# Performance work log

Hardware: AMD Instinct MI355X
Metric: run time of the kernel (lower is better)

The kernel has to match this reference:

```python
import jax, jax.numpy as jnp
import numpy as np

N = 100000   # nodes
E = 3200000  # edges (avg degree 32)
D_IN = 128
C = 64
EPS = 1e-5  # GraphNorm eps (PyG default)


def _graph_norm(x, alpha, gamma, beta):
    # GraphNorm over a single graph: all N nodes form one segment.
    mean = jnp.mean(x, axis=0, keepdims=True)            # [1, C]
    xc = x - alpha * mean                                # learnable mean-scale
    var = jnp.mean(xc * xc, axis=0, keepdims=True)       # [1, C]
    return gamma * xc * jax.lax.rsqrt(var + EPS) + beta


def _gcn_conv(x, W, bias, src, dst, dinv):
    # GCN with implicit self-loops: out = D^-1/2 (A+I) D^-1/2 (x W) + b
    xw = x @ W                                           # [N, C]
    coef = (dinv[src] * dinv[dst])[:, None]              # [E, 1]
    msg = xw[src] * coef                                 # [E, C] gather
    agg = jax.ops.segment_sum(msg, dst, num_segments=N)  # [N, C] scatter
    agg = agg + xw * (dinv * dinv)[:, None]              # self-loop term
    return agg + bias


def setup_inputs() -> dict:
    key = jax.random.key(0)
    ks = jax.random.split(key, 4)
    x = jax.random.normal(ks[0], (N, D_IN), dtype=jnp.float32)
    edge_index = jax.random.randint(ks[1], (2, E), 0, N, dtype=jnp.int64)
    W0 = jax.random.normal(ks[2], (D_IN, C), dtype=jnp.float32) * (1.0 / np.sqrt(D_IN))
    Ws = jax.random.normal(ks[3], (2, C, C), dtype=jnp.float32) * (1.0 / np.sqrt(C))
    b = jnp.zeros((3, C), dtype=jnp.float32)
    alpha = jnp.ones((3, C), dtype=jnp.float32)
    gamma = jnp.ones((3, C), dtype=jnp.float32)
    beta = jnp.zeros((3, C), dtype=jnp.float32)
    return {"x": x, "edge_index": edge_index, "W0": W0, "Ws": Ws,
            "b": b, "alpha": alpha, "gamma": gamma, "beta": beta}


def reference(x, edge_index, W0, Ws, b, alpha, gamma, beta):
    src, dst = edge_index[0], edge_index[1]
    deg = 1.0 + jax.ops.segment_sum(jnp.ones((E,), dtype=x.dtype), dst, num_segments=N)
    dinv = jax.lax.rsqrt(deg)                            # [N]
    h = _gcn_conv(x, W0, b[0], src, dst, dinv)
    h = _graph_norm(h, alpha[0], gamma[0], beta[0])      # dropout = identity (eval)
    for i in range(2):
        h = _gcn_conv(h, Ws[i], b[i + 1], src, dst, dinv)
        h = _graph_norm(h, alpha[i + 1], gamma[i + 1], beta[i + 1])
    return h
```

## Files before the change

kernel.cpp:

```cpp
#include <hip/hip_runtime.h>
#include <hip/hip_bf16.h>


#define EPS 1e-5f

__device__ __forceinline__ float bf_lo(unsigned u) {
    union { unsigned u; float f; } c; c.u = u << 16; return c.f;
}
__device__ __forceinline__ float bf_hi(unsigned u) {
    union { unsigned u; float f; } c; c.u = u & 0xffff0000u; return c.f;
}
__device__ __forceinline__ unsigned pack_bf2(float a, float b) {
    union { __hip_bfloat16 h; unsigned short u; } ca, cb;
    ca.h = __float2bfloat16(a);
    cb.h = __float2bfloat16(b);
    return (unsigned)ca.u | ((unsigned)cb.u << 16);
}

__global__ __launch_bounds__(256) void k_hist(const int* __restrict__ dst, int* __restrict__ hist,
                                              int E, int SEG, int NBKT) {
    __shared__ int h[2048];
    int t = threadIdx.x;
    for (int b = t; b < NBKT; b += 256) h[b] = 0;
    __syncthreads();
    int i0 = blockIdx.x * SEG, i1 = min(E, i0 + SEG);
    for (int i = i0 + t * 4; i < i1; i += 1024) {
        if (i + 3 < i1) {
            int4 d = *(const int4*)(dst + i);
            atomicAdd(&h[d.x >> 6], 1);
            atomicAdd(&h[d.y >> 6], 1);
            atomicAdd(&h[d.z >> 6], 1);
            atomicAdd(&h[d.w >> 6], 1);
        } else {
            for (int q = i; q < i1; ++q) atomicAdd(&h[dst[q] >> 6], 1);
        }
    }
    __syncthreads();
    for (int b = t; b < NBKT; b += 256) hist[blockIdx.x * NBKT + b] = h[b];
}

__global__ __launch_bounds__(256) void k_scanA(const int* __restrict__ hist, int* __restrict__ chunkScan,
                                               int* __restrict__ chunkTot, int NBKT, int SCAN_N) {
    __shared__ int ls[256];
    int t = threadIdx.x;
    int base = blockIdx.x * 1024 + t * 4;
    int v[4];
#pragma unroll
    for (int j = 0; j < 4; ++j) {
        int l = base + j;
        v[j] = 0;
        if (l < SCAN_N) {
            int blk = l & 255, bkt = l >> 8;
            v[j] = hist[blk * NBKT + bkt];
        }
    }
    int s = v[0] + v[1] + v[2] + v[3];
    ls[t] = s;
    __syncthreads();
    for (int off = 1; off < 256; off <<= 1) {
        int val = (t >= off) ? ls[t - off] : 0;
        __syncthreads();
        ls[t] += val;
        __syncthreads();
    }
    int run = ls[t] - s;
#pragma unroll
    for (int j = 0; j < 4; ++j) {
        chunkScan[base + j] = run;
        run += v[j];
    }
    if (t == 255) chunkTot[blockIdx.x] = ls[255];
}

__global__ void k_scanB(const int* __restrict__ chunkTot, int* __restrict__ chunkBase, int NCH) {
    __shared__ int s[512];
    int t = threadIdx.x;
    s[t] = (t < NCH) ? chunkTot[t] : 0;
    s[t + 256] = (t + 256 < NCH) ? chunkTot[t + 256] : 0;
    __syncthreads();
    for (int off = 1; off < 512; off <<= 1) {
        int a0 = (t >= off) ? s[t - off] : 0;
        int a1 = (t + 256 >= off) ? s[t + 256 - off] : 0;
        __syncthreads();
        s[t] += a0;
        s[t + 256] += a1;
        __syncthreads();
    }
    if (t < NCH) chunkBase[t] = t ? s[t - 1] : 0;
    if (t + 256 < NCH) chunkBase[t + 256] = s[t + 255];
}

__global__ __launch_bounds__(256) void k_scatter_part(const int* __restrict__ src, const int* __restrict__ dst,
                                                      const int* __restrict__ chunkScan,
                                                      const int* __restrict__ chunkBase,
                                                      int* __restrict__ packed, int E, int SEG, int NBKT) {
    __shared__ int cur[2048];
    int blk = blockIdx.x, t = threadIdx.x;
    for (int b = t; b < NBKT; b += 256) {
        int l = b * 256 + blk;
        cur[b] = chunkScan[l] + chunkBase[l >> 10];
    }
    __syncthreads();
    int i0 = blk * SEG, i1 = min(E, i0 + SEG);
    for (int i = i0 + t * 4; i < i1; i += 1024) {
        if (i + 3 < i1) {
            int4 d = *(const int4*)(dst + i);
            int4 s = *(const int4*)(src + i);
            int p;
            p = atomicAdd(&cur[d.x >> 6], 1); packed[p] = (int)(((unsigned)(d.x & 63) << 26) | (unsigned)s.x);
            p = atomicAdd(&cur[d.y >> 6], 1); packed[p] = (int)(((unsigned)(d.y & 63) << 26) | (unsigned)s.y);
            p = atomicAdd(&cur[d.z >> 6], 1); packed[p] = (int)(((unsigned)(d.z & 63) << 26) | (unsigned)s.z);
            p = atomicAdd(&cur[d.w >> 6], 1); packed[p] = (int)(((unsigned)(d.w & 63) << 26) | (unsigned)s.w);
        } else {
            for (int q = i; q < i1; ++q) {
                int dd = dst[q];
                int p = atomicAdd(&cur[dd >> 6], 1);
                packed[p] = (int)(((unsigned)(dd & 63) << 26) | (unsigned)src[q]);
            }
        }
    }
}

__global__ __launch_bounds__(256) void k_ellfill(const int* __restrict__ packed,
                                                 const int* __restrict__ chunkScan,
                                                 const int* __restrict__ chunkBase,
                                                 int* __restrict__ ell, int* __restrict__ cursor,
                                                 float* __restrict__ dinv,
                                                 int CAP, int NBKT, int N, int E) {
    __shared__ int ellLoc[64 * 96];
    __shared__ int cnt[64];
    int bkt = blockIdx.x, t = threadIdx.x;
    if (t < 64) cnt[t] = 0;
    __syncthreads();
    int l0 = bkt * 256;
    int bs = chunkScan[l0] + chunkBase[l0 >> 10];
    int be = E;
    if (bkt + 1 < NBKT) {
        int l1 = (bkt + 1) * 256;
        be = chunkScan[l1] + chunkBase[l1 >> 10];
    }
    for (int i = bs + t; i < be; i += 256) {
        unsigned p = (unsigned)packed[i];
        int s = (int)(p & 0x03FFFFFFu);
        int ld = (int)(p >> 26);
        int slot = atomicAdd(&cnt[ld], 1);
        if (slot < CAP) ellLoc[ld * CAP + slot] = s;
    }
    __syncthreads();
    int lo = bkt << 6;
    int total = 64 * CAP;
    for (int idx = t; idx < total; idx += 256) {
        int ld = idx / CAP;
        int s = idx - ld * CAP;
        if (lo + ld < N && s < min(cnt[ld], CAP))
            ell[(size_t)lo * CAP + idx] = ellLoc[idx];
    }
    if (t < 64 && lo + t < N) {
        int dg = min(cnt[t], CAP);
        cursor[lo + t] = (lo + t) * CAP + dg;
        dinv[lo + t] = rsqrtf(1.0f + (float)cnt[t]);
    }
}

__global__ __launch_bounds__(256) void k_cursor_init(int* cursor, int CAP, int n) {
    int i = blockIdx.x * 256 + threadIdx.x;
    if (i < n) cursor[i] = i * CAP;
}

__global__ __launch_bounds__(256) void k_fill_ell(const int* __restrict__ src, const int* __restrict__ dst,
                                                  int* cursor, int* __restrict__ ell, int E,
                                                  int lo, int hi) {
    int i = (blockIdx.x * 256 + threadIdx.x) * 4;
    if (i + 3 < E) {
        int4 d = *(const int4*)(dst + i);
        int4 s = *(const int4*)(src + i);
        if (d.x >= lo && d.x < hi) ell[atomicAdd(&cursor[d.x], 1)] = s.x;
        if (d.y >= lo && d.y < hi) ell[atomicAdd(&cursor[d.y], 1)] = s.y;
        if (d.z >= lo && d.z < hi) ell[atomicAdd(&cursor[d.z], 1)] = s.z;
        if (d.w >= lo && d.w < hi) ell[atomicAdd(&cursor[d.w], 1)] = s.w;
    } else {
        for (int t = i; t < E; ++t) {
            int d = dst[t];
            if (d >= lo && d < hi) ell[atomicAdd(&cursor[d], 1)] = src[t];
        }
    }
}

__global__ __launch_bounds__(256) void k_deg_dinv(const int* __restrict__ cursor, float* dinv, int CAP, int n) {
    int i = blockIdx.x * 256 + threadIdx.x;
    if (i < n) dinv[i] = rsqrtf(1.0f + (float)(cursor[i] - i * CAP));
}

template <int K, bool BIN>
__global__ __launch_bounds__(256) void gemm2(const void* __restrict__ in_, const float* __restrict__ Wp,
                                             const float* __restrict__ bb, const float* __restrict__ dinv,
                                             __hip_bfloat16* __restrict__ out, int N) {
    constexpr int ROWS = 64;
    __shared__ float xl[ROWS][K + 4];
    int tid = threadIdx.x;
    int c = tid & 63, rg = tid >> 6;
    int r0 = blockIdx.x * ROWS;

    if (!BIN) {
        const float* in = (const float*)in_;
        for (int i = tid; i < ROWS * (K / 4); i += 256) {
            int row = i / (K / 4);
            int kq = (i - row * (K / 4)) << 2;
            int grow = r0 + row;
            float4 v = make_float4(0.f, 0.f, 0.f, 0.f);
            if (grow < N) v = *(const float4*)&in[(size_t)grow * K + kq];
            *(float4*)&xl[row][kq] = v;
        }
    } else {
        const unsigned short* in = (const unsigned short*)in_;
        for (int i = tid; i < ROWS * (K / 8); i += 256) {
            int row = i / (K / 8);
            int k8 = (i - row * (K / 8)) << 3;
            int grow = r0 + row;
            uint4 v = make_uint4(0u, 0u, 0u, 0u);
            if (grow < N) v = *(const uint4*)(in + (size_t)grow * K + k8);
            float4 a = make_float4(bf_lo(v.x), bf_hi(v.x), bf_lo(v.y), bf_hi(v.y));
            float4 bq = make_float4(bf_lo(v.z), bf_hi(v.z), bf_lo(v.w), bf_hi(v.w));
            *(float4*)&xl[row][k8] = a;
            *(float4*)&xl[row][k8 + 4] = bq;
        }
    }
    __syncthreads();

    float acc[16];
#pragma unroll
    for (int j = 0; j < 16; ++j) acc[j] = 0.f;
    for (int k0 = 0; k0 < K; k0 += 4) {
        float w0 = Wp[(k0 + 0) * 64 + c];
        float w1 = Wp[(k0 + 1) * 64 + c];
        float w2 = Wp[(k0 + 2) * 64 + c];
        float w3 = Wp[(k0 + 3) * 64 + c];
#pragma unroll
        for (int j = 0; j < 16; ++j) {
            float4 x4 = *(const float4*)&xl[rg * 16 + j][k0];
            acc[j] = fmaf(x4.x, w0, acc[j]);
            acc[j] = fmaf(x4.y, w1, acc[j]);
            acc[j] = fmaf(x4.z, w2, acc[j]);
            acc[j] = fmaf(x4.w, w3, acc[j]);
        }
    }
    float bbv = bb ? bb[c] : 0.f;
#pragma unroll
    for (int j = 0; j < 16; ++j) {
        int row = r0 + rg * 16 + j;
        if (row < N) out[(size_t)row * 64 + c] = __float2bfloat16((acc[j] + bbv) * dinv[row]);
    }
}

template <bool OUT_BF16>
__global__ __launch_bounds__(256, 4) void k_pull(const int* __restrict__ cursor,
                                                 const int* __restrict__ ell,
                                                 const float* __restrict__ dinv,
                                                 const uint4* __restrict__ xwh,
                                                 const float* __restrict__ bias,
                                                 float* __restrict__ aggf,
                                                 __hip_bfloat16* __restrict__ aggh,
                                                 float* __restrict__ sums, float* __restrict__ sumsq,
                                                 int CAP, int N) {
    int tid = threadIdx.x;
    int lane = tid & 63;
    int g = lane >> 3;
    int cl = lane & 7;
    float bs[8];
#pragma unroll
    for (int k = 0; k < 8; ++k) bs[k] = bias[cl * 8 + k];
    float s_acc[8] = {0, 0, 0, 0, 0, 0, 0, 0};
    float q_acc[8] = {0, 0, 0, 0, 0, 0, 0, 0};

    int slot = (blockIdx.x * 4 + (tid >> 6)) * 8 + g;
    int nslots = gridDim.x * 32;
    for (int n = slot; n < N; n += nslots) {
        int beg = n * CAP, end = cursor[n];
        int last = end - 1;
        float acc[8];
        {
            uint4 v = xwh[(size_t)n * 8 + cl];
            acc[0] = bf_lo(v.x); acc[1] = bf_hi(v.x);
            acc[2] = bf_lo(v.y); acc[3] = bf_hi(v.y);
            acc[4] = bf_lo(v.z); acc[5] = bf_hi(v.z);
            acc[6] = bf_lo(v.w); acc[7] = bf_hi(v.w);
        }
        int i = beg;
        for (; i + 8 <= end; i += 8) {
            int4 ia = *(const int4*)&ell[i];
            int4 ib = *(const int4*)&ell[i + 4];
            uint4 vv[8];
            vv[0] = xwh[(size_t)ia.x * 8 + cl];
            vv[1] = xwh[(size_t)ia.y * 8 + cl];
            vv[2] = xwh[(size_t)ia.z * 8 + cl];
            vv[3] = xwh[(size_t)ia.w * 8 + cl];
            vv[4] = xwh[(size_t)ib.x * 8 + cl];
            vv[5] = xwh[(size_t)ib.y * 8 + cl];
            vv[6] = xwh[(size_t)ib.z * 8 + cl];
            vv[7] = xwh[(size_t)ib.w * 8 + cl];
#pragma unroll
            for (int k = 0; k < 8; ++k) {
                acc[0] += bf_lo(vv[k].x); acc[1] += bf_hi(vv[k].x);
                acc[2] += bf_lo(vv[k].y); acc[3] += bf_hi(vv[k].y);
                acc[4] += bf_lo(vv[k].z); acc[5] += bf_hi(vv[k].z);
                acc[6] += bf_lo(vv[k].w); acc[7] += bf_hi(vv[k].w);
            }
        }
        if (i < end) {
            int4 ia = *(const int4*)&ell[i];
            int4 ib = *(const int4*)&ell[i + 4];
            int ss[8];
            ss[0] = ia.x; ss[1] = ia.y; ss[2] = ia.z; ss[3] = ia.w;
            ss[4] = ib.x; ss[5] = ib.y; ss[6] = ib.z; ss[7] = ib.w;
#pragma unroll
            for (int k = 0; k < 8; ++k) ss[k] = (i + k <= last) ? ss[k] : 0;
            uint4 vv[8];
#pragma unroll
            for (int k = 0; k < 8; ++k) vv[k] = xwh[(size_t)ss[k] * 8 + cl];
#pragma unroll
            for (int k = 0; k < 8; ++k) {
                if (i + k > last) { vv[k].x = 0; vv[k].y = 0; vv[k].z = 0; vv[k].w = 0; }
                acc[0] += bf_lo(vv[k].x); acc[1] += bf_hi(vv[k].x);
                acc[2] += bf_lo(vv[k].y); acc[3] += bf_hi(vv[k].y);
                acc[4] += bf_lo(vv[k].z); acc[5] += bf_hi(vv[k].z);
                acc[6] += bf_lo(vv[k].w); acc[7] += bf_hi(vv[k].w);
            }
        }
        float dn = dinv[n];
        float r[8];
#pragma unroll
        for (int k = 0; k < 8; ++k) {
            r[k] = dn * acc[k] + bs[k];
            s_acc[k] += r[k];
            q_acc[k] += r[k] * r[k];
        }
        if (OUT_BF16) {
            uint4 o;
            o.x = pack_bf2(r[0], r[1]);
            o.y = pack_bf2(r[2], r[3]);
            o.z = pack_bf2(r[4], r[5]);
            o.w = pack_bf2(r[6], r[7]);
            *(uint4*)((unsigned short*)aggh + (size_t)n * 64 + cl * 8) = o;
        } else {
            float4* d4 = (float4*)(aggf + (size_t)n * 64 + cl * 8);
            d4[0] = make_float4(r[0], r[1], r[2], r[3]);
            d4[1] = make_float4(r[4], r[5], r[6], r[7]);
        }
    }

    __shared__ float lsum[256][9], lsq[256][9];
#pragma unroll
    for (int k = 0; k < 8; ++k) { lsum[tid][k] = s_acc[k]; lsq[tid][k] = q_acc[k]; }
    __syncthreads();
    if (tid < 64) {
        int cl_t = tid >> 3, k_t = tid & 7;
        float s = 0.f, q = 0.f;
        for (int j = 0; j < 32; ++j) {
            int l = cl_t + 8 * j;
            s += lsum[l][k_t];
            q += lsq[l][k_t];
        }
        atomicAdd(&sums[tid], s);
        atomicAdd(&sumsq[tid], q);
    }
}

__global__ void k_params2(float* __restrict__ sums, float* __restrict__ sumsq,
                          const float* __restrict__ alpha, const float* __restrict__ gamma,
                          const float* __restrict__ beta, const float* __restrict__ W,
                          float* __restrict__ scale, float* __restrict__ shift,
                          float* __restrict__ Wp, float* __restrict__ bb, int N) {
    __shared__ float ssc[64], ssh[64];
    int c = threadIdx.x;
    float invN = 1.0f / (float)N;
    float m = sums[c] * invN;
    float ex2 = sumsq[c] * invN;
    float a = alpha[c];
    float var = ex2 - 2.0f * a * m * m + a * a * m * m;
    float sc = gamma[c] * rsqrtf(var + EPS);
    float sh = beta[c] - sc * a * m;
    scale[c] = sc;
    shift[c] = sh;
    ssc[c] = sc;
    ssh[c] = sh;
    sums[c] = 0.f;
    sumsq[c] = 0.f;
    __syncthreads();
    if (W) {
        float acc = 0.f;
        for (int k = 0; k < 64; ++k) {
            float w = W[k * 64 + c];
            Wp[k * 64 + c] = ssc[k] * w;
            acc += ssh[k] * w;
        }
        bb[c] = acc;
    }
}

__global__ __launch_bounds__(256) void k_final(float* __restrict__ out, const float* __restrict__ scale,
                                               const float* __restrict__ shift, int n64) {
    int i = blockIdx.x * 256 + threadIdx.x;
    if (i < n64) out[i] = scale[i & 63] * out[i] + shift[i & 63];
}

extern "C" void kernel_launch(void* const* d_in, const int* in_sizes, int n_in,
                              void* d_out, int out_size, void* d_ws, size_t ws_size,
                              hipStream_t stream) {
    const float* x     = (const float*)d_in[0];
    const int*   ei    = (const int*)d_in[1];
    const float* W0    = (const float*)d_in[2];
    const float* Wsp   = (const float*)d_in[3];
    const float* b     = (const float*)d_in[4];
    const float* alpha = (const float*)d_in[5];
    const float* gamma = (const float*)d_in[6];
    const float* beta  = (const float*)d_in[7];

    const int N = in_sizes[0] / 128;
    const int E = in_sizes[1] / 2;
    const int* src = ei;
    const int* dst = ei + E;

    float* aggf = (float*)d_out;

    const int Na = ((N + 63) / 64) * 64;
    float* ws = (float*)d_ws;
    size_t off = 0;
    float* dinv  = ws + off; off += Na;
    __hip_bfloat16* xwh = (__hip_bfloat16*)(ws + off); off += (size_t)Na * 32;
    __hip_bfloat16* hb  = (__hip_bfloat16*)(ws + off); off += (size_t)Na * 32;
    float* sums  = ws + off; off += 64;
    float* sumsq = ws + off; off += 64;
    float* scbuf = ws + off; off += 64;
    float* shbuf = ws + off; off += 64;
    float* Wp    = ws + off; off += 64 * 64;
    float* bbv   = ws + off; off += 64;
    int* cursor  = (int*)(ws + off); off += Na;

    int CAP = 96;
    while (CAP > 72 && (off + (size_t)N * CAP + 8) * 4 > ws_size) CAP -= 8;
    int* ell = (int*)(ws + off); off += (size_t)N * CAP + 8;

    const int n64 = N * 64;
    const int RB = (N + 63) / 64;
    const int NB = (N + 255) / 256;
    const int PB = (N + 63) / 64;

    const int NBKT = (N + 63) >> 6;
    const int NSEG = 256;
    int SEG = ((E + NSEG - 1) / NSEG + 3) & ~3;
    const int SCAN_N = NBKT * 256;
    const int NCH = (SCAN_N + 1023) / 1024;
    int* packed    = (int*)xwh;
    int* hist      = (int*)hb;
    int* chunkScan = hist + (size_t)NSEG * NBKT;
    int* chunkTot  = chunkScan + (size_t)NCH * 1024;
    int* chunkBase = chunkTot + NCH;
    bool fast_build = (NBKT <= 2048) && (NCH <= 512) && (N < (1 << 26)) &&
                      ((size_t)E <= (size_t)Na * 32) &&
                      ((size_t)NSEG * NBKT + (size_t)NCH * 1024 + 2 * NCH <= (size_t)Na * 32);

    if (fast_build) {
        k_hist<<<NSEG, 256, 0, stream>>>(dst, hist, E, SEG, NBKT);
        k_scanA<<<NCH, 256, 0, stream>>>(hist, chunkScan, chunkTot, NBKT, SCAN_N);
        k_scanB<<<1, 256, 0, stream>>>(chunkTot, chunkBase, NCH);
        k_scatter_part<<<NSEG, 256, 0, stream>>>(src, dst, chunkScan, chunkBase, packed, E, SEG, NBKT);
        k_ellfill<<<NBKT, 256, 0, stream>>>(packed, chunkScan, chunkBase, ell, cursor, dinv,
                                            CAP, NBKT, N, E);
    } else {
        k_cursor_init<<<NB, 256, 0, stream>>>(cursor, CAP, N);
        const int NCHUNK = 10;
        int cs = (N + NCHUNK - 1) / NCHUNK;
        const int EB4 = (E / 4 + 255) / 256;
        for (int c = 0; c < NCHUNK; ++c) {
            int lo = c * cs, hi = min(N, lo + cs);
            k_fill_ell<<<EB4, 256, 0, stream>>>(src, dst, cursor, ell, E, lo, hi);
        }
        k_deg_dinv<<<NB, 256, 0, stream>>>(cursor, dinv, CAP, N);
    }

    hipMemsetAsync(sums, 0, 128 * sizeof(float), stream);

    for (int layer = 0; layer < 3; ++layer) {
        if (layer == 0) {
            gemm2<128, false><<<RB, 256, 0, stream>>>(x, W0, nullptr, dinv, xwh, N);
        } else {
            gemm2<64, true><<<RB, 256, 0, stream>>>(hb, Wp, bbv, dinv, xwh, N);
        }
        if (layer < 2) {
            k_pull<true><<<PB, 256, 0, stream>>>(cursor, ell, dinv, (const uint4*)xwh,
                                                 b + layer * 64, nullptr, hb,
                                                 sums, sumsq, CAP, N);
        } else {
            k_pull<false><<<PB, 256, 0, stream>>>(cursor, ell, dinv, (const uint4*)xwh,
                                                  b + layer * 64, aggf, nullptr,
                                                  sums, sumsq, CAP, N);
        }
        const float* Wnext = (layer < 2) ? (Wsp + (size_t)layer * 64 * 64) : nullptr;
        k_params2<<<1, 64, 0, stream>>>(sums, sumsq, alpha + layer * 64, gamma + layer * 64,
                                        beta + layer * 64, Wnext, scbuf, shbuf, Wp, bbv, N);
    }
    k_final<<<(n64 + 255) / 256, 256, 0, stream>>>(aggf, scbuf, shbuf, n64);
}
```

Measured before the change: 412.0 us.

## Replace scalar FMA GEMMs with bf16 MFMA kernels and pre-transposed bf16 weights

The per-layer dense transforms move from an LDS-tiled scalar fp32 FMA kernel to a kernel using 16x16x32 bf16 MFMA instructions. A-fragments are loaded straight from global memory, with no shared-memory staging, and fp32 input is converted to bf16 in registers. Weights are stored transposed as bf16 by a new pack kernel for layer 0 and by k_params2 for later layers. This targets compute time in the GEMMs. In exchange, the first layer's input and all weights lose precision to bf16, and one extra tiny kernel launch is added.

```diff
diff --git a/kernel.cpp b/kernel.cpp
--- a/kernel.cpp
+++ b/kernel.cpp
@@ -3,6 +3,9 @@
 
 
 #define EPS 1e-5f
+
+typedef __attribute__((ext_vector_type(8))) short bf16x8;
+typedef __attribute__((ext_vector_type(4))) float f32x4;
 
 __device__ __forceinline__ float bf_lo(unsigned u) {
     union { unsigned u; float f; } c; c.u = u << 16; return c.f;
@@ -15,6 +18,9 @@
     ca.h = __float2bfloat16(a);
     cb.h = __float2bfloat16(b);
     return (unsigned)ca.u | ((unsigned)cb.u << 16);
+}
+__device__ __forceinline__ short bfb(float f) {
+    union { __hip_bfloat16 h; short s; } u; u.h = __float2bfloat16(f); return u.s;
 }
 
 __global__ __launch_bounds__(256) void k_hist(const int* __restrict__ dst, int* __restrict__ hist,
@@ -191,65 +197,59 @@
     if (i < n) dinv[i] = rsqrtf(1.0f + (float)(cursor[i] - i * CAP));
 }
 
-template <int K, bool BIN>
-__global__ __launch_bounds__(256) void gemm2(const void* __restrict__ in_, const float* __restrict__ Wp,
-                                             const float* __restrict__ bb, const float* __restrict__ dinv,
-                                             __hip_bfloat16* __restrict__ out, int N) {
-    constexpr int ROWS = 64;
-    __shared__ float xl[ROWS][K + 4];
+template <int K, bool AFP32>
+__global__ __launch_bounds__(256) void gemm_mfma(const void* __restrict__ in_,
+                                                 const unsigned short* __restrict__ Wb,
+                                                 const float* __restrict__ bbv,
+                                                 const float* __restrict__ dinv,
+                                                 __hip_bfloat16* __restrict__ out, int N) {
+    constexpr int NC = K / 32;
     int tid = threadIdx.x;
-    int c = tid & 63, rg = tid >> 6;
-    int r0 = blockIdx.x * ROWS;
-
-    if (!BIN) {
-        const float* in = (const float*)in_;
-        for (int i = tid; i < ROWS * (K / 4); i += 256) {
-            int row = i / (K / 4);
-            int kq = (i - row * (K / 4)) << 2;
-            int grow = r0 + row;
-            float4 v = make_float4(0.f, 0.f, 0.f, 0.f);
-            if (grow < N) v = *(const float4*)&in[(size_t)grow * K + kq];
-            *(float4*)&xl[row][kq] = v;
-        }
-    } else {
-        const unsigned short* in = (const unsigned short*)in_;
-        for (int i = tid; i < ROWS * (K / 8); i += 256) {
-            int row = i / (K / 8);
-            int k8 = (i - row * (K / 8)) << 3;
-            int grow = r0 + row;
-            uint4 v = make_uint4(0u, 0u, 0u, 0u);
-            if (grow < N) v = *(const uint4*)(in + (size_t)grow * K + k8);
-            float4 a = make_float4(bf_lo(v.x), bf_hi(v.x), bf_lo(v.y), bf_hi(v.y));
-            float4 bq = make_float4(bf_lo(v.z), bf_hi(v.z), bf_lo(v.w), bf_hi(v.w));
-            *(float4*)&xl[row][k8] = a;
-            *(float4*)&xl[row][k8 + 4] = bq;
-        }
-    }
-    __syncthreads();
-
-    float acc[16];
-#pragma unroll
-    for (int j = 0; j < 16; ++j) acc[j] = 0.f;
-    for (int k0 = 0; k0 < K; k0 += 4) {
-        float w0 = Wp[(k0 + 0) * 64 + c];
-        float w1 = Wp[(k0 + 1) * 64 + c];
-        float w2 = Wp[(k0 + 2) * 64 + c];
-        float w3 = Wp[(k0 + 3) * 64 + c];
-#pragma unroll
-        for (int j = 0; j < 16; ++j) {
-            float4 x4 = *(const float4*)&xl[rg * 16 + j][k0];
-            acc[j] = fmaf(x4.x, w0, acc[j]);
-            acc[j] = fmaf(x4.y, w1, acc[j]);
-            acc[j] = fmaf(x4.z, w2, acc[j]);
-            acc[j] = fmaf(x4.w, w3, acc[j]);
-        }
-    }
-    float bbv = bb ? bb[c] : 0.f;
-#pragma unroll
-    for (int j = 0; j < 16; ++j) {
-        int row = r0 + rg * 16 + j;
-        if (row < N) out[(size_t)row * 64 + c] = __float2bfloat16((acc[j] + bbv) * dinv[row]);
-    }
+    int lane = tid & 63, w = tid >> 6;
+    int r0 = blockIdx.x * 64;
+    int col = w * 16 + (lane & 15);
+    int kg = lane >> 4;
+
+    bf16x8 bfrag[NC];
+#pragma unroll
+    for (int kc = 0; kc < NC; ++kc)
+        bfrag[kc] = *(const bf16x8*)(Wb + (size_t)col * K + kc * 32 + kg * 8);
+    float bbc = bbv ? bbv[col] : 0.f;
+
+#pragma unroll 1
+    for (int rt = 0; rt < 4; ++rt) {
+        int arow = r0 + rt * 16 + (lane & 15);
+        int arow_c = min(arow, N - 1);
+        f32x4 acc = {0.f, 0.f, 0.f, 0.f};
+#pragma unroll
+        for (int kc = 0; kc < NC; ++kc) {
+            bf16x8 afrag;
+            if (AFP32) {
+                const float* in = (const float*)in_ + (size_t)arow_c * K + kc * 32 + kg * 8;
+                float4 lo = *(const float4*)in;
+                float4 hi = *(const float4*)(in + 4);
+                union { short s[8]; bf16x8 v; } cv;
+                cv.s[0] = bfb(lo.x); cv.s[1] = bfb(lo.y); cv.s[2] = bfb(lo.z); cv.s[3] = bfb(lo.w);
+                cv.s[4] = bfb(hi.x); cv.s[5] = bfb(hi.y); cv.s[6] = bfb(hi.z); cv.s[7] = bfb(hi.w);
+                afrag = cv.v;
+            } else {
+                const unsigned short* in = (const unsigned short*)in_;
+                afrag = *(const bf16x8*)(in + (size_t)arow_c * K + kc * 32 + kg * 8);
+            }
+            acc = __builtin_amdgcn_mfma_f32_16x16x32_bf16(afrag, bfrag[kc], acc, 0, 0, 0);
+        }
+#pragma unroll
+        for (int j = 0; j < 4; ++j) {
+            int row = r0 + rt * 16 + kg * 4 + j;
+            if (row < N)
+                out[(size_t)row * 64 + col] = __float2bfloat16((acc[j] + bbc) * dinv[row]);
+        }
+    }
+}
+
+__global__ void k_packW0(const float* __restrict__ W0, unsigned short* __restrict__ Wb) {
+    int c = threadIdx.x;
+    for (int k = 0; k < 128; ++k) Wb[c * 128 + k] = (unsigned short)bfb(W0[k * 64 + c]);
 }
 
 template <bool OUT_BF16>
@@ -369,7 +369,7 @@
                           const float* __restrict__ alpha, const float* __restrict__ gamma,
                           const float* __restrict__ beta, const float* __restrict__ W,
                           float* __restrict__ scale, float* __restrict__ shift,
-                          float* __restrict__ Wp, float* __restrict__ bb, int N) {
+                          unsigned short* __restrict__ Wb, float* __restrict__ bb, int N) {
     __shared__ float ssc[64], ssh[64];
     int c = threadIdx.x;
     float invN = 1.0f / (float)N;
@@ -390,7 +390,7 @@
         float acc = 0.f;
         for (int k = 0; k < 64; ++k) {
             float w = W[k * 64 + c];
-            Wp[k * 64 + c] = ssc[k] * w;
+            Wb[c * 64 + k] = (unsigned short)bfb(ssc[k] * w);
             acc += ssh[k] * w;
         }
         bb[c] = acc;
@@ -432,7 +432,7 @@
     float* sumsq = ws + off; off += 64;
     float* scbuf = ws + off; off += 64;
     float* shbuf = ws + off; off += 64;
-    float* Wp    = ws + off; off += 64 * 64;
+    unsigned short* Wb = (unsigned short*)(ws + off); off += 4096;
     float* bbv   = ws + off; off += 64;
     int* cursor  = (int*)(ws + off); off += Na;
 
@@ -479,12 +479,13 @@
     }
 
     hipMemsetAsync(sums, 0, 128 * sizeof(float), stream);
+    k_packW0<<<1, 64, 0, stream>>>(W0, Wb);
 
     for (int layer = 0; layer < 3; ++layer) {
         if (layer == 0) {
-            gemm2<128, false><<<RB, 256, 0, stream>>>(x, W0, nullptr, dinv, xwh, N);
+            gemm_mfma<128, true><<<RB, 256, 0, stream>>>(x, Wb, nullptr, dinv, xwh, N);
         } else {
-            gemm2<64, true><<<RB, 256, 0, stream>>>(hb, Wp, bbv, dinv, xwh, N);
+            gemm_mfma<64, false><<<RB, 256, 0, stream>>>(hb, Wb, bbv, dinv, xwh, N);
         }
         if (layer < 2) {
             k_pull<true><<<PB, 256, 0, stream>>>(cursor, ell, dinv, (const uint4*)xwh,
@@ -497,7 +498,7 @@
         }
         const float* Wnext = (layer < 2) ? (Wsp + (size_t)layer * 64 * 64) : nullptr;
         k_params2<<<1, 64, 0, stream>>>(sums, sumsq, alpha + layer * 64, gamma + layer * 64,
-                                        beta + layer * 64, Wnext, scbuf, shbuf, Wp, bbv, N);
+                                        beta + layer * 64, Wnext, scbuf, shbuf, Wb, bbv, N);
     }
     k_final<<<(n64 + 255) / 256, 256, 0, stream>>>(aggf, scbuf, shbuf, n64);
 }
```

After: 386.3 us (median of 2 runs). 6.2% less time.
